# Kernel optimization log

Hardware: AMD Instinct MI355X
Metric: run time of the kernel (lower is better)

## Reference

```python
import jax, jax.numpy as jnp
import numpy as np

B, TE, TD, H, D = 8, 2048, 256, 128, 128


def setup_inputs() -> dict:
    key = jax.random.key(0)
    k1, k2, k3, k4, k5 = jax.random.split(key, 5)
    he = lambda k, shape: jax.random.normal(k, shape, dtype=jnp.float32) * jnp.sqrt(2.0 / shape[0])
    return {
        "encoder_out_seq": jax.random.normal(k1, (B, TE, H), dtype=jnp.float32),
        "decoder_out_seq": jax.random.normal(k2, (B, TD, D), dtype=jnp.float32),
        "W_a": he(k3, (H, H)),
        "U_a": he(k4, (D, H)),
        "V_a": he(k5, (H, 1)),
    }


def reference(encoder_out_seq, decoder_out_seq, W_a, U_a, V_a):
    # Precompute encoder and decoder projections once (the TF code redundantly
    # recomputes enc@W_a every decoder step inside backend.rnn).
    Wenc = jnp.einsum('bth,hk->btk', encoder_out_seq, W_a)      # [B,Te,H]
    Udec = jnp.einsum('bjd,dk->bjk', decoder_out_seq, U_a)     # [B,Td,H]
    # Additive (Bahdanau) scores: v^T tanh(W s_i + U h_j)
    scores = jnp.einsum('bjtk,k->bjt',
                        jnp.tanh(Wenc[:, None, :, :] + Udec[:, :, None, :]),
                        V_a[:, 0])                              # [B,Td,Te]
    e_outputs = jax.nn.softmax(scores, axis=-1)                 # [B,Td,Te]
    c_outputs = jnp.einsum('bjt,bth->bjh', e_outputs, encoder_out_seq)  # [B,Td,H]
    return c_outputs, e_outputs
```

## Files before the change

kernel.cpp:

```cpp
#include <hip/hip_runtime.h>
#include <stdint.h>

#define B  8
#define TE 2048
#define TD 256
#define H  128

__global__ __launch_bounds__(256) void proj_kernel(
    const float* __restrict__ enc, const float* __restrict__ dec,
    const float* __restrict__ Wa,  const float* __restrict__ Ua,
    float* __restrict__ EgT, float* __restrict__ Fg) {
  __shared__ float Ls[32 * 132];
  const float C2 = 2.8853900817779268f;
  int tid = threadIdx.x;
  int bid = blockIdx.x;
  bool isE = (bid < 512);
  int rbase = (isE ? bid : bid - 512) * 32;
  const float* in = isE ? enc : dec;
  const float* Mg = isE ? Wa : Ua;
  int hq = tid & 31, rq = tid >> 5;
  int h0 = hq * 4, r0 = rq * 4;
  const float* rowp = in + (size_t)(rbase + r0) * H;
  const float* wp = Mg + h0;
  float4 a0{0,0,0,0}, a1{0,0,0,0}, a2{0,0,0,0}, a3{0,0,0,0};
  #pragma unroll 4
  for (int k = 0; k < 128; ++k) {
    float4 wv = *(const float4*)(wp + (size_t)k * H);
    float r0v = rowp[k];
    float r1v = rowp[k + H];
    float r2v = rowp[k + 2 * H];
    float r3v = rowp[k + 3 * H];
    a0.x += r0v * wv.x; a0.y += r0v * wv.y; a0.z += r0v * wv.z; a0.w += r0v * wv.w;
    a1.x += r1v * wv.x; a1.y += r1v * wv.y; a1.z += r1v * wv.z; a1.w += r1v * wv.w;
    a2.x += r2v * wv.x; a2.y += r2v * wv.y; a2.z += r2v * wv.z; a2.w += r2v * wv.w;
    a3.x += r3v * wv.x; a3.y += r3v * wv.y; a3.z += r3v * wv.z; a3.w += r3v * wv.w;
  }
  float4 e0, e1, e2, e3;
  e0.x = __builtin_amdgcn_exp2f(a0.x * C2); e0.y = __builtin_amdgcn_exp2f(a0.y * C2);
  e0.z = __builtin_amdgcn_exp2f(a0.z * C2); e0.w = __builtin_amdgcn_exp2f(a0.w * C2);
  e1.x = __builtin_amdgcn_exp2f(a1.x * C2); e1.y = __builtin_amdgcn_exp2f(a1.y * C2);
  e1.z = __builtin_amdgcn_exp2f(a1.z * C2); e1.w = __builtin_amdgcn_exp2f(a1.w * C2);
  e2.x = __builtin_amdgcn_exp2f(a2.x * C2); e2.y = __builtin_amdgcn_exp2f(a2.y * C2);
  e2.z = __builtin_amdgcn_exp2f(a2.z * C2); e2.w = __builtin_amdgcn_exp2f(a2.w * C2);
  e3.x = __builtin_amdgcn_exp2f(a3.x * C2); e3.y = __builtin_amdgcn_exp2f(a3.y * C2);
  e3.z = __builtin_amdgcn_exp2f(a3.z * C2); e3.w = __builtin_amdgcn_exp2f(a3.w * C2);
  if (isE) {
    *(float4*)&Ls[(r0 + 0) * 132 + h0] = e0;
    *(float4*)&Ls[(r0 + 1) * 132 + h0] = e1;
    *(float4*)&Ls[(r0 + 2) * 132 + h0] = e2;
    *(float4*)&Ls[(r0 + 3) * 132 + h0] = e3;
    __syncthreads();
    int b_e = rbase >> 11, t_in = rbase & 2047;
    int tb = t_in >> 6, toff = t_in & 63;
    float* dst = EgT + ((size_t)(b_e * 32 + tb) * 128) * 64 + toff;
    #pragma unroll
    for (int jj = 0; jj < 16; ++jj) {
      int idx = jj * 256 + tid;
      int r = idx & 31, k = idx >> 5;
      dst[(size_t)k * 64 + r] = Ls[r * 132 + k];
    }
  } else {
    int b_f = rbase >> 8, j_in = rbase & 255;
    float* dst = Fg + ((size_t)(b_f * TD + j_in + r0)) * H + h0;
    *(float4*)(dst + 0 * H) = e0;
    *(float4*)(dst + 1 * H) = e1;
    *(float4*)(dst + 2 * H) = e2;
    *(float4*)(dst + 3 * H) = e3;
  }
}

__global__ __launch_bounds__(256) void scores_kernel(
    const float* __restrict__ EgT, const float* __restrict__ Fg,
    const float* __restrict__ Va, float* __restrict__ scores) {
  int tid = threadIdx.x;
  int tc = blockIdx.x, jt = blockIdx.y, b = blockIdx.z;
  int lane = tid & 63, w = tid >> 6;
  int tb = tc * 4 + w;
  int j0 = jt * 8;
  const float* Ep = EgT + ((size_t)(b * 32 + tb) * 128) * 64 + lane;
  const float4* Fp = (const float4*)(Fg + (size_t)(b * TD + j0) * H);
  const float4* vp = (const float4*)Va;
  float s[8] = {0.f, 0.f, 0.f, 0.f, 0.f, 0.f, 0.f, 0.f};
  float V1 = 0.f;
  for (int kc = 0; kc < 16; ++kc) {
    const float* ep = Ep + kc * 512;
    float ek[8];
    #pragma unroll
    for (int q = 0; q < 8; ++q) ek[q] = ep[q * 64];
    float4 v0 = vp[kc * 2], v1 = vp[kc * 2 + 1];
    V1 += v0.x + v0.y + v0.z + v0.w + v1.x + v1.y + v1.z + v1.w;
    const float4* fp = Fp + kc * 2;
    #pragma unroll
    for (int j = 0; j < 8; ++j) {
      float4 f0 = fp[j * 32];
      float4 f1 = fp[j * 32 + 1];
      s[j] += v0.x * __builtin_amdgcn_rcpf(fmaf(ek[0], f0.x, 1.0f));
      s[j] += v0.y * __builtin_amdgcn_rcpf(fmaf(ek[1], f0.y, 1.0f));
      s[j] += v0.z * __builtin_amdgcn_rcpf(fmaf(ek[2], f0.z, 1.0f));
      s[j] += v0.w * __builtin_amdgcn_rcpf(fmaf(ek[3], f0.w, 1.0f));
      s[j] += v1.x * __builtin_amdgcn_rcpf(fmaf(ek[4], f1.x, 1.0f));
      s[j] += v1.y * __builtin_amdgcn_rcpf(fmaf(ek[5], f1.y, 1.0f));
      s[j] += v1.z * __builtin_amdgcn_rcpf(fmaf(ek[6], f1.z, 1.0f));
      s[j] += v1.w * __builtin_amdgcn_rcpf(fmaf(ek[7], f1.w, 1.0f));
    }
  }
  int t = tb * 64 + lane;
  float* srow = scores + (size_t)(b * TD + j0) * TE + t;
  #pragma unroll
  for (int j = 0; j < 8; ++j)
    srow[(size_t)j * TE] = V1 - 2.0f * s[j];
}

__global__ __launch_bounds__(256) void softmax_kernel(
    const float* __restrict__ scores, float* __restrict__ eout) {
  __shared__ float red[4];
  int r = blockIdx.x, tid = threadIdx.x;
  const float* row = scores + (size_t)r * TE;
  float4 a = ((const float4*)row)[tid];
  float4 c = ((const float4*)row)[tid + 256];
  float m = fmaxf(fmaxf(fmaxf(a.x, a.y), fmaxf(a.z, a.w)),
                  fmaxf(fmaxf(c.x, c.y), fmaxf(c.z, c.w)));
  #pragma unroll
  for (int off = 32; off > 0; off >>= 1) m = fmaxf(m, __shfl_xor(m, off));
  int w = tid >> 6;
  if ((tid & 63) == 0) red[w] = m;
  __syncthreads();
  m = fmaxf(fmaxf(red[0], red[1]), fmaxf(red[2], red[3]));
  const float L2E = 1.4426950408889634f;
  a.x = __builtin_amdgcn_exp2f((a.x - m) * L2E);
  a.y = __builtin_amdgcn_exp2f((a.y - m) * L2E);
  a.z = __builtin_amdgcn_exp2f((a.z - m) * L2E);
  a.w = __builtin_amdgcn_exp2f((a.w - m) * L2E);
  c.x = __builtin_amdgcn_exp2f((c.x - m) * L2E);
  c.y = __builtin_amdgcn_exp2f((c.y - m) * L2E);
  c.z = __builtin_amdgcn_exp2f((c.z - m) * L2E);
  c.w = __builtin_amdgcn_exp2f((c.w - m) * L2E);
  float s = a.x + a.y + a.z + a.w + c.x + c.y + c.z + c.w;
  #pragma unroll
  for (int off = 32; off > 0; off >>= 1) s += __shfl_xor(s, off);
  __syncthreads();
  if ((tid & 63) == 0) red[w] = s;
  __syncthreads();
  s = red[0] + red[1] + red[2] + red[3];
  float inv = 1.0f / s;
  a.x *= inv; a.y *= inv; a.z *= inv; a.w *= inv;
  c.x *= inv; c.y *= inv; c.z *= inv; c.w *= inv;
  float* orow = eout + (size_t)r * TE;
  ((float4*)orow)[tid] = a;
  ((float4*)orow)[tid + 256] = c;
}

__global__ __launch_bounds__(512) void context_kernel(
    const float* __restrict__ enc, const float* __restrict__ e,
    float* __restrict__ part) {
  int tid = threadIdx.x;
  int jt = blockIdx.x, tch = blockIdx.y, b = blockIdx.z;
  int hg = tid & 15, jg = tid >> 4;
  int h0 = hg * 8;
  int j = jt * 128 + jg * 4;
  int t0 = tch * 128;
  const float* e0p  = e + (size_t)(b * TD + j) * TE + t0;
  const float* encp = enc + ((size_t)b * TE + t0) * H + h0;
  float4 acc[4][2];
  #pragma unroll
  for (int p = 0; p < 4; ++p) {
    acc[p][0] = float4{0.f, 0.f, 0.f, 0.f};
    acc[p][1] = float4{0.f, 0.f, 0.f, 0.f};
  }
  #pragma unroll 2
  for (int t4 = 0; t4 < 128; t4 += 4) {
    float4 pj[4];
    #pragma unroll
    for (int p = 0; p < 4; ++p)
      pj[p] = *(const float4*)(e0p + (size_t)p * TE + t4);
    #pragma unroll
    for (int i = 0; i < 4; ++i) {
      const float* er = encp + (size_t)(t4 + i) * H;
      float4 ev0 = *(const float4*)er;
      float4 ev1 = *(const float4*)(er + 4);
      #pragma unroll
      for (int p = 0; p < 4; ++p) {
        float pv = (i == 0) ? pj[p].x : (i == 1) ? pj[p].y : (i == 2) ? pj[p].z : pj[p].w;
        acc[p][0].x += pv * ev0.x; acc[p][0].y += pv * ev0.y;
        acc[p][0].z += pv * ev0.z; acc[p][0].w += pv * ev0.w;
        acc[p][1].x += pv * ev1.x; acc[p][1].y += pv * ev1.y;
        acc[p][1].z += pv * ev1.z; acc[p][1].w += pv * ev1.w;
      }
    }
  }
  #pragma unroll
  for (int p = 0; p < 4; ++p) {
    float* dst = part + (size_t)tch * (B * TD * H) + (size_t)(b * TD + j + p) * H + h0;
    *(float4*)dst = acc[p][0];
    *(float4*)(dst + 4) = acc[p][1];
  }
}

__global__ __launch_bounds__(256) void reduce_kernel(
    const float4* __restrict__ part, float4* __restrict__ outc) {
  int i = blockIdx.x * 256 + threadIdx.x;
  float4 a = part[i];
  #pragma unroll
  for (int q = 1; q < 16; ++q) {
    float4 p = part[(size_t)q * 65536 + i];
    a.x += p.x; a.y += p.y; a.z += p.z; a.w += p.w;
  }
  outc[i] = a;
}

extern "C" void kernel_launch(void* const* d_in, const int* in_sizes, int n_in,
                              void* d_out, int out_size, void* d_ws, size_t ws_size,
                              hipStream_t stream) {
  (void)in_sizes; (void)n_in; (void)out_size; (void)ws_size;
  const float* enc = (const float*)d_in[0];
  const float* dec = (const float*)d_in[1];
  const float* Wa  = (const float*)d_in[2];
  const float* Ua  = (const float*)d_in[3];
  const float* Va  = (const float*)d_in[4];

  float* ws     = (float*)d_ws;
  float* EgT    = ws;
  float* Fg     = EgT + (size_t)B * TE * H;
  float* scores = Fg + (size_t)B * TD * H;
  float* outc = (float*)d_out;
  float* oute = outc + (size_t)B * TD * H;

  proj_kernel<<<dim3(576), 256, 0, stream>>>(enc, dec, Wa, Ua, EgT, Fg);
  scores_kernel<<<dim3(8, 32, 8), 256, 0, stream>>>(EgT, Fg, Va, scores);
  softmax_kernel<<<dim3(B * TD), 256, 0, stream>>>(scores, oute);
  context_kernel<<<dim3(2, 16, 8), 512, 0, stream>>>(enc, oute, scores);
  reduce_kernel<<<dim3(256), 256, 0, stream>>>((const float4*)scores, (float4*)outc);
}
```

Measured before the change: 201.2 us.

## Fuse scores, softmax and context into one kernel per 4 decoder rows

Replaces four kernels (scores, softmax, context, partial-sum reduce) with one fused kernel. Each block computes scores for 4 decoder rows across all encoder steps and keeps them in shared memory, then does the softmax and the context product, reducing the context partial sums in shared memory. This removes the global round trips for the scores and partial buffers, plus three launches. In exchange, each block now handles only 4 rows instead of 8, so every Fg/EgT load is reused across fewer decoder rows. The grid is 512 blocks using 32KB of shared memory each, and each block reads the full encoder sequence for its batch.

New measurement: 175.4 us. 1.15x faster.

```diff
diff --git a/kernel.cpp b/kernel.cpp
--- a/kernel.cpp
+++ b/kernel.cpp
@@ -69,143 +69,114 @@
   }
 }
 
-__global__ __launch_bounds__(256) void scores_kernel(
+__global__ __launch_bounds__(512) void fused_kernel(
     const float* __restrict__ EgT, const float* __restrict__ Fg,
-    const float* __restrict__ Va, float* __restrict__ scores) {
+    const float* __restrict__ Va,  const float* __restrict__ enc,
+    float* __restrict__ oute, float* __restrict__ outc) {
+  __shared__ float S[4 * 2048];
+  __shared__ float red[16];
   int tid = threadIdx.x;
-  int tc = blockIdx.x, jt = blockIdx.y, b = blockIdx.z;
+  int jt = blockIdx.x, b = blockIdx.y;
+  int j0 = jt * 4;
   int lane = tid & 63, w = tid >> 6;
-  int tb = tc * 4 + w;
-  int j0 = jt * 8;
-  const float* Ep = EgT + ((size_t)(b * 32 + tb) * 128) * 64 + lane;
+  const float4* vp = (const float4*)Va;
+  float V1 = 0.f;
+  #pragma unroll
+  for (int q = 0; q < 32; ++q) { float4 v = vp[q]; V1 += v.x + v.y + v.z + v.w; }
+
   const float4* Fp = (const float4*)(Fg + (size_t)(b * TD + j0) * H);
-  const float4* vp = (const float4*)Va;
-  float s[8] = {0.f, 0.f, 0.f, 0.f, 0.f, 0.f, 0.f, 0.f};
-  float V1 = 0.f;
-  for (int kc = 0; kc < 16; ++kc) {
-    const float* ep = Ep + kc * 512;
-    float ek[8];
-    #pragma unroll
-    for (int q = 0; q < 8; ++q) ek[q] = ep[q * 64];
-    float4 v0 = vp[kc * 2], v1 = vp[kc * 2 + 1];
-    V1 += v0.x + v0.y + v0.z + v0.w + v1.x + v1.y + v1.z + v1.w;
-    const float4* fp = Fp + kc * 2;
-    #pragma unroll
-    for (int j = 0; j < 8; ++j) {
-      float4 f0 = fp[j * 32];
-      float4 f1 = fp[j * 32 + 1];
-      s[j] += v0.x * __builtin_amdgcn_rcpf(fmaf(ek[0], f0.x, 1.0f));
-      s[j] += v0.y * __builtin_amdgcn_rcpf(fmaf(ek[1], f0.y, 1.0f));
-      s[j] += v0.z * __builtin_amdgcn_rcpf(fmaf(ek[2], f0.z, 1.0f));
-      s[j] += v0.w * __builtin_amdgcn_rcpf(fmaf(ek[3], f0.w, 1.0f));
-      s[j] += v1.x * __builtin_amdgcn_rcpf(fmaf(ek[4], f1.x, 1.0f));
-      s[j] += v1.y * __builtin_amdgcn_rcpf(fmaf(ek[5], f1.y, 1.0f));
-      s[j] += v1.z * __builtin_amdgcn_rcpf(fmaf(ek[6], f1.z, 1.0f));
-      s[j] += v1.w * __builtin_amdgcn_rcpf(fmaf(ek[7], f1.w, 1.0f));
-    }
-  }
-  int t = tb * 64 + lane;
-  float* srow = scores + (size_t)(b * TD + j0) * TE + t;
-  #pragma unroll
-  for (int j = 0; j < 8; ++j)
-    srow[(size_t)j * TE] = V1 - 2.0f * s[j];
-}
-
-__global__ __launch_bounds__(256) void softmax_kernel(
-    const float* __restrict__ scores, float* __restrict__ eout) {
-  __shared__ float red[4];
-  int r = blockIdx.x, tid = threadIdx.x;
-  const float* row = scores + (size_t)r * TE;
-  float4 a = ((const float4*)row)[tid];
-  float4 c = ((const float4*)row)[tid + 256];
-  float m = fmaxf(fmaxf(fmaxf(a.x, a.y), fmaxf(a.z, a.w)),
-                  fmaxf(fmaxf(c.x, c.y), fmaxf(c.z, c.w)));
-  #pragma unroll
-  for (int off = 32; off > 0; off >>= 1) m = fmaxf(m, __shfl_xor(m, off));
-  int w = tid >> 6;
-  if ((tid & 63) == 0) red[w] = m;
-  __syncthreads();
-  m = fmaxf(fmaxf(red[0], red[1]), fmaxf(red[2], red[3]));
-  const float L2E = 1.4426950408889634f;
-  a.x = __builtin_amdgcn_exp2f((a.x - m) * L2E);
-  a.y = __builtin_amdgcn_exp2f((a.y - m) * L2E);
-  a.z = __builtin_amdgcn_exp2f((a.z - m) * L2E);
-  a.w = __builtin_amdgcn_exp2f((a.w - m) * L2E);
-  c.x = __builtin_amdgcn_exp2f((c.x - m) * L2E);
-  c.y = __builtin_amdgcn_exp2f((c.y - m) * L2E);
-  c.z = __builtin_amdgcn_exp2f((c.z - m) * L2E);
-  c.w = __builtin_amdgcn_exp2f((c.w - m) * L2E);
-  float s = a.x + a.y + a.z + a.w + c.x + c.y + c.z + c.w;
-  #pragma unroll
-  for (int off = 32; off > 0; off >>= 1) s += __shfl_xor(s, off);
-  __syncthreads();
-  if ((tid & 63) == 0) red[w] = s;
-  __syncthreads();
-  s = red[0] + red[1] + red[2] + red[3];
-  float inv = 1.0f / s;
-  a.x *= inv; a.y *= inv; a.z *= inv; a.w *= inv;
-  c.x *= inv; c.y *= inv; c.z *= inv; c.w *= inv;
-  float* orow = eout + (size_t)r * TE;
-  ((float4*)orow)[tid] = a;
-  ((float4*)orow)[tid + 256] = c;
-}
-
-__global__ __launch_bounds__(512) void context_kernel(
-    const float* __restrict__ enc, const float* __restrict__ e,
-    float* __restrict__ part) {
-  int tid = threadIdx.x;
-  int jt = blockIdx.x, tch = blockIdx.y, b = blockIdx.z;
-  int hg = tid & 15, jg = tid >> 4;
-  int h0 = hg * 8;
-  int j = jt * 128 + jg * 4;
-  int t0 = tch * 128;
-  const float* e0p  = e + (size_t)(b * TD + j) * TE + t0;
-  const float* encp = enc + ((size_t)b * TE + t0) * H + h0;
-  float4 acc[4][2];
-  #pragma unroll
-  for (int p = 0; p < 4; ++p) {
-    acc[p][0] = float4{0.f, 0.f, 0.f, 0.f};
-    acc[p][1] = float4{0.f, 0.f, 0.f, 0.f};
-  }
-  #pragma unroll 2
-  for (int t4 = 0; t4 < 128; t4 += 4) {
-    float4 pj[4];
-    #pragma unroll
-    for (int p = 0; p < 4; ++p)
-      pj[p] = *(const float4*)(e0p + (size_t)p * TE + t4);
-    #pragma unroll
-    for (int i = 0; i < 4; ++i) {
-      const float* er = encp + (size_t)(t4 + i) * H;
-      float4 ev0 = *(const float4*)er;
-      float4 ev1 = *(const float4*)(er + 4);
+  for (int it = 0; it < 4; ++it) {
+    int tb = w + 8 * it;
+    const float* Ep = EgT + ((size_t)(b * 32 + tb) * 128) * 64 + lane;
+    float s0 = 0.f, s1 = 0.f, s2 = 0.f, s3 = 0.f;
+    for (int kc = 0; kc < 16; ++kc) {
+      const float* ep = Ep + kc * 512;
+      float ek[8];
       #pragma unroll
-      for (int p = 0; p < 4; ++p) {
-        float pv = (i == 0) ? pj[p].x : (i == 1) ? pj[p].y : (i == 2) ? pj[p].z : pj[p].w;
-        acc[p][0].x += pv * ev0.x; acc[p][0].y += pv * ev0.y;
-        acc[p][0].z += pv * ev0.z; acc[p][0].w += pv * ev0.w;
-        acc[p][1].x += pv * ev1.x; acc[p][1].y += pv * ev1.y;
-        acc[p][1].z += pv * ev1.z; acc[p][1].w += pv * ev1.w;
+      for (int q = 0; q < 8; ++q) ek[q] = ep[q * 64];
+      float4 v0 = vp[kc * 2], v1 = vp[kc * 2 + 1];
+      const float4* fp = Fp + kc * 2;
+      #pragma unroll
+      for (int j = 0; j < 4; ++j) {
+        float4 f0 = fp[j * 32];
+        float4 f1 = fp[j * 32 + 1];
+        float a;
+        a  = v0.x * __builtin_amdgcn_rcpf(fmaf(ek[0], f0.x, 1.0f));
+        a += v0.y * __builtin_amdgcn_rcpf(fmaf(ek[1], f0.y, 1.0f));
+        a += v0.z * __builtin_amdgcn_rcpf(fmaf(ek[2], f0.z, 1.0f));
+        a += v0.w * __builtin_amdgcn_rcpf(fmaf(ek[3], f0.w, 1.0f));
+        a += v1.x * __builtin_amdgcn_rcpf(fmaf(ek[4], f1.x, 1.0f));
+        a += v1.y * __builtin_amdgcn_rcpf(fmaf(ek[5], f1.y, 1.0f));
+        a += v1.z * __builtin_amdgcn_rcpf(fmaf(ek[6], f1.z, 1.0f));
+        a += v1.w * __builtin_amdgcn_rcpf(fmaf(ek[7], f1.w, 1.0f));
+        if (j == 0) s0 += a; else if (j == 1) s1 += a; else if (j == 2) s2 += a; else s3 += a;
       }
     }
-  }
-  #pragma unroll
-  for (int p = 0; p < 4; ++p) {
-    float* dst = part + (size_t)tch * (B * TD * H) + (size_t)(b * TD + j + p) * H + h0;
-    *(float4*)dst = acc[p][0];
-    *(float4*)(dst + 4) = acc[p][1];
-  }
-}
-
-__global__ __launch_bounds__(256) void reduce_kernel(
-    const float4* __restrict__ part, float4* __restrict__ outc) {
-  int i = blockIdx.x * 256 + threadIdx.x;
-  float4 a = part[i];
-  #pragma unroll
-  for (int q = 1; q < 16; ++q) {
-    float4 p = part[(size_t)q * 65536 + i];
-    a.x += p.x; a.y += p.y; a.z += p.z; a.w += p.w;
-  }
-  outc[i] = a;
+    int t = tb * 64 + lane;
+    S[0 * 2048 + t] = V1 - 2.0f * s0;
+    S[1 * 2048 + t] = V1 - 2.0f * s1;
+    S[2 * 2048 + t] = V1 - 2.0f * s2;
+    S[3 * 2048 + t] = V1 - 2.0f * s3;
+  }
+  __syncthreads();
+
+  int j = w >> 1, half = w & 1;
+  int tb2 = half * 1024 + lane;
+  float x[16];
+  #pragma unroll
+  for (int q = 0; q < 16; ++q) x[q] = S[j * 2048 + tb2 + q * 64];
+  float m = x[0];
+  #pragma unroll
+  for (int q = 1; q < 16; ++q) m = fmaxf(m, x[q]);
+  #pragma unroll
+  for (int off = 32; off > 0; off >>= 1) m = fmaxf(m, __shfl_xor(m, off));
+  if (lane == 0) red[w] = m;
+  __syncthreads();
+  m = fmaxf(red[j * 2], red[j * 2 + 1]);
+  const float L2E = 1.4426950408889634f;
+  float sum = 0.f;
+  #pragma unroll
+  for (int q = 0; q < 16; ++q) {
+    x[q] = __builtin_amdgcn_exp2f((x[q] - m) * L2E);
+    sum += x[q];
+  }
+  #pragma unroll
+  for (int off = 32; off > 0; off >>= 1) sum += __shfl_xor(sum, off);
+  if (lane == 0) red[8 + w] = sum;
+  __syncthreads();
+  float inv = 1.0f / (red[8 + j * 2] + red[8 + j * 2 + 1]);
+  float* orow = oute + (size_t)(b * TD + j0 + j) * TE;
+  #pragma unroll
+  for (int q = 0; q < 16; ++q) {
+    float e = x[q] * inv;
+    int t = tb2 + q * 64;
+    orow[t] = e;
+    S[t * 4 + j] = e;
+  }
+  __syncthreads();
+
+  int hq = tid & 31, slice = tid >> 5;
+  const float* encp = enc + ((size_t)b * TE + slice * 128) * H + hq * 4;
+  float4 acc0{0,0,0,0}, acc1{0,0,0,0}, acc2{0,0,0,0}, acc3{0,0,0,0};
+  #pragma unroll 4
+  for (int t = 0; t < 128; ++t) {
+    float4 ev = *(const float4*)(encp + (size_t)t * H);
+    float4 e4 = *(const float4*)&S[(slice * 128 + t) * 4];
+    acc0.x += e4.x * ev.x; acc0.y += e4.x * ev.y; acc0.z += e4.x * ev.z; acc0.w += e4.x * ev.w;
+    acc1.x += e4.y * ev.x; acc1.y += e4.y * ev.y; acc1.z += e4.y * ev.z; acc1.w += e4.y * ev.w;
+    acc2.x += e4.z * ev.x; acc2.y += e4.z * ev.y; acc2.z += e4.z * ev.z; acc2.w += e4.z * ev.w;
+    acc3.x += e4.w * ev.x; acc3.y += e4.w * ev.y; acc3.z += e4.w * ev.z; acc3.w += e4.w * ev.w;
+  }
+  __syncthreads();
+  *(float4*)&S[slice * 512 + 0 * 128 + hq * 4] = acc0;
+  *(float4*)&S[slice * 512 + 1 * 128 + hq * 4] = acc1;
+  *(float4*)&S[slice * 512 + 2 * 128 + hq * 4] = acc2;
+  *(float4*)&S[slice * 512 + 3 * 128 + hq * 4] = acc3;
+  __syncthreads();
+  float r = 0.f;
+  #pragma unroll
+  for (int sl = 0; sl < 16; ++sl) r += S[sl * 512 + tid];
+  outc[(size_t)(b * TD + j0 + (tid >> 7)) * H + (tid & 127)] = r;
 }
 
 extern "C" void kernel_launch(void* const* d_in, const int* in_sizes, int n_in,
@@ -218,16 +189,12 @@
   const float* Ua  = (const float*)d_in[3];
   const float* Va  = (const float*)d_in[4];
 
-  float* ws     = (float*)d_ws;
-  float* EgT    = ws;
-  float* Fg     = EgT + (size_t)B * TE * H;
-  float* scores = Fg + (size_t)B * TD * H;
+  float* ws  = (float*)d_ws;
+  float* EgT = ws;
+  float* Fg  = EgT + (size_t)B * TE * H;
   float* outc = (float*)d_out;
   float* oute = outc + (size_t)B * TD * H;
 
   proj_kernel<<<dim3(576), 256, 0, stream>>>(enc, dec, Wa, Ua, EgT, Fg);
-  scores_kernel<<<dim3(8, 32, 8), 256, 0, stream>>>(EgT, Fg, Va, scores);
-  softmax_kernel<<<dim3(B * TD), 256, 0, stream>>>(scores, oute);
-  context_kernel<<<dim3(2, 16, 8), 512, 0, stream>>>(enc, oute, scores);
-  reduce_kernel<<<dim3(256), 256, 0, stream>>>((const float4*)scores, (float4*)outc);
+  fused_kernel<<<dim3(64, 8), 512, 0, stream>>>(EgT, Fg, Va, enc, oute, outc);
 }
```
